# Kernel tuning notes

Measured on AMD Instinct MI355X. Metric: run time of the kernel, lower is better.

The kernel has to match this reference:

```python
import jax, jax.numpy as jnp
import numpy as np

# dims mirroring the torch module: dim=32 (MVN), omega=8, d_head=n_embd//n_head
B, T, E, DH = 8, 2048, 1024, 32
OMEGA, DIM = 8, 32
M = OMEGA * DIM  # 256 random features (omega concatenated N(0, I_dim) samples)


def setup_inputs() -> dict:
    key = jax.random.key(0)
    ks = jax.random.split(key, 8)
    s = 1.0 / np.sqrt(E).astype(np.float32)  # torch Linear-like init scale
    return {
        "x": jax.random.normal(ks[0], (B, T, E), jnp.float32),
        "Wq": jax.random.normal(ks[1], (E, DH), jnp.float32) * s,
        "bq": jax.random.normal(ks[2], (DH,), jnp.float32) * s,
        "Wk": jax.random.normal(ks[3], (E, DH), jnp.float32) * s,
        "bk": jax.random.normal(ks[4], (DH,), jnp.float32) * s,
        "Wv": jax.random.normal(ks[5], (E, DH), jnp.float32) * s,
        "bv": jax.random.normal(ks[6], (DH,), jnp.float32) * s,
        # random-feature matrix: omega stacked samples from N(0, I_DIM) -> [M, DH]
        "w": jax.random.normal(ks[7], (M, DH), jnp.float32),
    }


def reference(x, Wq, bq, Wk, bk, Wv, bv, w):
    # projections (as in Head.forward)
    q = x @ Wq + bq  # [B,T,DH]
    k = x @ Wk + bk  # [B,T,DH]
    v = x @ Wv + bv  # computed but unused, exactly as in the source
    del v
    # Aprox_softmax (FAVOR+-style hyperbolic random features), vectorized per token
    z = k + q                                          # [B,T,DH]
    zsqr = jnp.sum(k * k, -1) + jnp.sum(q * q, -1)     # [B,T]  (per-token norms)
    A = jnp.exp(-0.5 * zsqr)                           # [B,T]
    cosH = jnp.cosh(jnp.einsum('btd,md->btm', z, w))   # [B,T,M]
    R = A[..., None] * cosH                            # [B,T,M]
    return R
```

## Files before the change

### kernel.cpp

```cpp
#include <hip/hip_runtime.h>
#include <cstdint>

#define E_DIM   1024
#define DH      32
#define M_FEAT  256
#define BT      16384

typedef __attribute__((ext_vector_type(8))) short bf16x8;
typedef __attribute__((ext_vector_type(4))) float f32x4;

#define WP_H_OFF 0
#define WP_L_OFF (64*1024)
#define WF_H_OFF (2*64*1024)
#define WF_L_OFF (2*64*1024 + 256*32)

__device__ __forceinline__ void split_bf16(float f, short& h, short& l) {
    unsigned u = __builtin_bit_cast(unsigned, f);
    unsigned hr = (u + 0x7FFFu + ((u >> 16) & 1u)) & 0xFFFF0000u;
    h = (short)(hr >> 16);
    float fh = __builtin_bit_cast(float, hr);
    float d = f - fh;
    unsigned v = __builtin_bit_cast(unsigned, d);
    l = (short)((v + 0x7FFFu + ((v >> 16) & 1u)) >> 16);
}

__device__ __forceinline__ unsigned pack2(short a, short b) {
    return ((unsigned)(unsigned short)a) | (((unsigned)(unsigned short)b) << 16);
}

__global__ __launch_bounds__(256) void k_prep(
    const float* __restrict__ Wq, const float* __restrict__ Wk,
    const float* __restrict__ w, short* __restrict__ ws)
{
    int idx = blockIdx.x * 256 + threadIdx.x;
    short h[4], l[4];
    if (idx < 16384) {
        int n = idx >> 8, kq = idx & 255;
        const float* src = (n < 32) ? (Wq + n) : (Wk + (n - 32));
#pragma unroll
        for (int j = 0; j < 4; ++j) split_bf16(src[(kq * 4 + j) * DH], h[j], l[j]);
        uint2 ph = make_uint2(pack2(h[0], h[1]), pack2(h[2], h[3]));
        uint2 pl = make_uint2(pack2(l[0], l[1]), pack2(l[2], l[3]));
        *(uint2*)(ws + WP_H_OFF + n * 1024 + kq * 4) = ph;
        *(uint2*)(ws + WP_L_OFF + n * 1024 + kq * 4) = pl;
    } else if (idx < 16384 + 2048) {
        int j2 = idx - 16384;
        int n = j2 >> 3, kq = j2 & 7;
#pragma unroll
        for (int j = 0; j < 4; ++j) split_bf16(w[n * DH + kq * 4 + j], h[j], l[j]);
        uint2 ph = make_uint2(pack2(h[0], h[1]), pack2(h[2], h[3]));
        uint2 pl = make_uint2(pack2(l[0], l[1]), pack2(l[2], l[3]));
        *(uint2*)(ws + WF_H_OFF + n * DH + kq * 4) = ph;
        *(uint2*)(ws + WF_L_OFF + n * DH + kq * 4) = pl;
    }
}

#define XS 72
#define QS 68
#define ZS 40

__global__ __launch_bounds__(256) void k_main(
    const float* __restrict__ x, const float* __restrict__ bq,
    const float* __restrict__ bk, const short* __restrict__ ws,
    float* __restrict__ out)
{
    __shared__ __align__(16) short xh_s[32 * XS];
    __shared__ __align__(16) short xl_s[32 * XS];
    __shared__ __align__(16) float qk_f[32 * QS];
    __shared__ __align__(16) short zh_s[32 * ZS];
    __shared__ __align__(16) short zl_s[32 * ZS];
    __shared__ float lnA_f[32];

    const int tid  = threadIdx.x;
    const int lane = tid & 63;
    const int wv   = __builtin_amdgcn_readfirstlane(tid >> 6);
    const int ln15 = lane & 15;
    const int g    = lane >> 4;
    const long t0  = (long)blockIdx.x * 32;

    const short* wp_h = ws + WP_H_OFF;
    const short* wp_l = ws + WP_L_OFF;
    const short* wf_h = ws + WF_H_OFF;
    const short* wf_l = ws + WF_L_OFF;

    const int kq = tid & 15;
    const int mr = tid >> 4;

    f32x4 acc0 = {0.f, 0.f, 0.f, 0.f};
    f32x4 acc1 = {0.f, 0.f, 0.f, 0.f};

    const int nrow = wv * 16 + ln15;

    float4 st0 = *(const float4*)(x + (t0 + mr) * E_DIM + kq * 4);
    float4 st1 = *(const float4*)(x + (t0 + mr + 16) * E_DIM + kq * 4);

    for (int c = 0; c < 16; ++c) {
        __syncthreads();
        {
            short h0,h1,h2,h3, l0,l1,l2,l3;
            split_bf16(st0.x,h0,l0); split_bf16(st0.y,h1,l1);
            split_bf16(st0.z,h2,l2); split_bf16(st0.w,h3,l3);
            *(uint2*)&xh_s[mr * XS + kq * 4] = make_uint2(pack2(h0,h1), pack2(h2,h3));
            *(uint2*)&xl_s[mr * XS + kq * 4] = make_uint2(pack2(l0,l1), pack2(l2,l3));
            split_bf16(st1.x,h0,l0); split_bf16(st1.y,h1,l1);
            split_bf16(st1.z,h2,l2); split_bf16(st1.w,h3,l3);
            *(uint2*)&xh_s[(mr+16) * XS + kq * 4] = make_uint2(pack2(h0,h1), pack2(h2,h3));
            *(uint2*)&xl_s[(mr+16) * XS + kq * 4] = make_uint2(pack2(l0,l1), pack2(l2,l3));
        }
        __syncthreads();
        if (c < 15) {
            st0 = *(const float4*)(x + (t0 + mr) * E_DIM + (c+1)*64 + kq * 4);
            st1 = *(const float4*)(x + (t0 + mr + 16) * E_DIM + (c+1)*64 + kq * 4);
        }
#pragma unroll
        for (int s = 0; s < 2; ++s) {
            const int kb = c * 64 + s * 32;
            bf16x8 bh = *(const bf16x8*)(wp_h + nrow * 1024 + kb + g * 8);
            bf16x8 bl = *(const bf16x8*)(wp_l + nrow * 1024 + kb + g * 8);
            bf16x8 a0h = *(const bf16x8*)&xh_s[ln15 * XS + s * 32 + g * 8];
            bf16x8 a0l = *(const bf16x8*)&xl_s[ln15 * XS + s * 32 + g * 8];
            bf16x8 a1h = *(const bf16x8*)&xh_s[(ln15 + 16) * XS + s * 32 + g * 8];
            bf16x8 a1l = *(const bf16x8*)&xl_s[(ln15 + 16) * XS + s * 32 + g * 8];
            acc0 = __builtin_amdgcn_mfma_f32_16x16x32_bf16(a0h, bh, acc0, 0, 0, 0);
            acc0 = __builtin_amdgcn_mfma_f32_16x16x32_bf16(a0h, bl, acc0, 0, 0, 0);
            acc0 = __builtin_amdgcn_mfma_f32_16x16x32_bf16(a0l, bh, acc0, 0, 0, 0);
            acc1 = __builtin_amdgcn_mfma_f32_16x16x32_bf16(a1h, bh, acc1, 0, 0, 0);
            acc1 = __builtin_amdgcn_mfma_f32_16x16x32_bf16(a1h, bl, acc1, 0, 0, 0);
            acc1 = __builtin_amdgcn_mfma_f32_16x16x32_bf16(a1l, bh, acc1, 0, 0, 0);
        }
    }

    {
        const float bias = (nrow < 32) ? bq[nrow] : bk[nrow - 32];
#pragma unroll
        for (int r = 0; r < 4; ++r) {
            qk_f[(g * 4 + r) * QS + nrow]      = acc0[r] + bias;
            qk_f[(16 + g * 4 + r) * QS + nrow] = acc1[r] + bias;
        }
    }
    __syncthreads();

    {
        const int tok = tid >> 3, grp = tid & 7;
        float4 qv = *(const float4*)&qk_f[tok * QS + grp * 4];
        float4 kv = *(const float4*)&qk_f[tok * QS + 32 + grp * 4];
        float z0 = qv.x + kv.x, z1 = qv.y + kv.y, z2 = qv.z + kv.z, z3 = qv.w + kv.w;
        float p = qv.x*qv.x + qv.y*qv.y + qv.z*qv.z + qv.w*qv.w
                + kv.x*kv.x + kv.y*kv.y + kv.z*kv.z + kv.w*kv.w;
        short h0,h1,h2,h3, l0,l1,l2,l3;
        split_bf16(z0,h0,l0); split_bf16(z1,h1,l1);
        split_bf16(z2,h2,l2); split_bf16(z3,h3,l3);
        *(uint2*)&zh_s[tok * ZS + grp * 4] = make_uint2(pack2(h0,h1), pack2(h2,h3));
        *(uint2*)&zl_s[tok * ZS + grp * 4] = make_uint2(pack2(l0,l1), pack2(l2,l3));
        p += __shfl_xor(p, 1);
        p += __shfl_xor(p, 2);
        p += __shfl_xor(p, 4);
        if (grp == 0) lnA_f[tok] = -0.5f * p;
    }
    __syncthreads();

    f32x4 facc[4][2];
#pragma unroll
    for (int i = 0; i < 4; ++i)
#pragma unroll
        for (int mt = 0; mt < 2; ++mt) facc[i][mt] = (f32x4){0.f,0.f,0.f,0.f};

    bf16x8 a_h[2], a_l[2];
#pragma unroll
    for (int mt = 0; mt < 2; ++mt) {
        a_h[mt] = *(const bf16x8*)&zh_s[(mt * 16 + ln15) * ZS + g * 8];
        a_l[mt] = *(const bf16x8*)&zl_s[(mt * 16 + ln15) * ZS + g * 8];
    }
#pragma unroll
    for (int i = 0; i < 4; ++i) {
        const int nf = (wv * 4 + i) * 16 + ln15;
        bf16x8 bh = *(const bf16x8*)(wf_h + nf * DH + g * 8);
        bf16x8 bl = *(const bf16x8*)(wf_l + nf * DH + g * 8);
#pragma unroll
        for (int mt = 0; mt < 2; ++mt) {
            facc[i][mt] = __builtin_amdgcn_mfma_f32_16x16x32_bf16(a_h[mt], bh, facc[i][mt], 0, 0, 0);
            facc[i][mt] = __builtin_amdgcn_mfma_f32_16x16x32_bf16(a_h[mt], bl, facc[i][mt], 0, 0, 0);
            facc[i][mt] = __builtin_amdgcn_mfma_f32_16x16x32_bf16(a_l[mt], bh, facc[i][mt], 0, 0, 0);
        }
    }

    float lnAv[2][4];
#pragma unroll
    for (int mt = 0; mt < 2; ++mt)
#pragma unroll
        for (int r = 0; r < 4; ++r) lnAv[mt][r] = lnA_f[mt * 16 + g * 4 + r];

#pragma unroll
    for (int i = 0; i < 4; ++i) {
        const int n = (wv * 4 + i) * 16 + ln15;
#pragma unroll
        for (int mt = 0; mt < 2; ++mt) {
#pragma unroll
            for (int r = 0; r < 4; ++r) {
                float s = facc[i][mt][r];
                float R = 0.5f * (__expf(lnAv[mt][r] + s) + __expf(lnAv[mt][r] - s));
                out[(t0 + mt * 16 + g * 4 + r) * M_FEAT + n] = R;
            }
        }
    }
}

extern "C" void kernel_launch(void* const* d_in, const int* in_sizes, int n_in,
                              void* d_out, int out_size, void* d_ws, size_t ws_size,
                              hipStream_t stream) {
    const float* x  = (const float*)d_in[0];
    const float* Wq = (const float*)d_in[1];
    const float* bq = (const float*)d_in[2];
    const float* Wk = (const float*)d_in[3];
    const float* bk = (const float*)d_in[4];
    const float* w  = (const float*)d_in[7];
    float* out = (float*)d_out;
    short* ws  = (short*)d_ws;

    k_prep<<<dim3(72), dim3(256), 0, stream>>>(Wq, Wk, w, ws);
    k_main<<<dim3(BT / 32), dim3(256), 0, stream>>>(x, bq, bk, ws, out);
}
```

Baseline: 132.9 us.

## Halve token tile, double-buffer x in LDS, pre-swizzle weights into MFMA fragment layout

The main kernel now processes 16 tokens per block instead of 32, which doubles the grid to 1024 blocks. The x tile is double-buffered in shared memory, so one barrier per chunk is dropped and the bf16 split of the next chunk runs after the MFMAs. The prep kernel transposes the projection weights through LDS and writes them in per-lane fragment order, so each wave reads B fragments as contiguous coalesced 16-byte loads. The trade-off is that each block now re-reads the full projection weights for only 16 tokens, doubling weight traffic per token.

```diff
diff --git a/kernel.cpp b/kernel.cpp
--- a/kernel.cpp
+++ b/kernel.cpp
@@ -10,9 +10,9 @@
 typedef __attribute__((ext_vector_type(4))) float f32x4;
 
 #define WP_H_OFF 0
-#define WP_L_OFF (64*1024)
-#define WF_H_OFF (2*64*1024)
-#define WF_L_OFF (2*64*1024 + 256*32)
+#define WP_L_OFF 65536
+#define WF_H_OFF 131072
+#define WF_L_OFF (131072 + 8192)
 
 __device__ __forceinline__ void split_bf16(float f, short& h, short& l) {
     unsigned u = __builtin_bit_cast(unsigned, f);
@@ -32,29 +32,52 @@
     const float* __restrict__ Wq, const float* __restrict__ Wk,
     const float* __restrict__ w, short* __restrict__ ws)
 {
-    int idx = blockIdx.x * 256 + threadIdx.x;
-    short h[4], l[4];
-    if (idx < 16384) {
-        int n = idx >> 8, kq = idx & 255;
-        const float* src = (n < 32) ? (Wq + n) : (Wk + (n - 32));
-#pragma unroll
-        for (int j = 0; j < 4; ++j) split_bf16(src[(kq * 4 + j) * DH], h[j], l[j]);
-        uint2 ph = make_uint2(pack2(h[0], h[1]), pack2(h[2], h[3]));
-        uint2 pl = make_uint2(pack2(l[0], l[1]), pack2(l[2], l[3]));
-        *(uint2*)(ws + WP_H_OFF + n * 1024 + kq * 4) = ph;
-        *(uint2*)(ws + WP_L_OFF + n * 1024 + kq * 4) = pl;
-    } else if (idx < 16384 + 2048) {
-        int j2 = idx - 16384;
-        int n = j2 >> 3, kq = j2 & 7;
-#pragma unroll
-        for (int j = 0; j < 4; ++j) split_bf16(w[n * DH + kq * 4 + j], h[j], l[j]);
-        uint2 ph = make_uint2(pack2(h[0], h[1]), pack2(h[2], h[3]));
-        uint2 pl = make_uint2(pack2(l[0], l[1]), pack2(l[2], l[3]));
-        *(uint2*)(ws + WF_H_OFF + n * DH + kq * 4) = ph;
-        *(uint2*)(ws + WF_L_OFF + n * DH + kq * 4) = pl;
-    }
-}
-
+    __shared__ float wlds[128 * 36];
+    const int b = blockIdx.x, tid = threadIdx.x;
+    if (b < 16) {
+        const float* __restrict__ src = (b < 8) ? Wq : Wk;
+        const int k0 = (b & 7) * 128;
+        const int nbase = (b < 8) ? 0 : 32;
+#pragma unroll
+        for (int it = 0; it < 4; ++it) {
+            int f = it * 256 + tid;
+            int k = f >> 3, c4 = f & 7;
+            float4 v = *(const float4*)(src + (size_t)(k0 + k) * DH + c4 * 4);
+            *(float4*)&wlds[k * 36 + c4 * 4] = v;
+        }
+        __syncthreads();
+        const int n = tid >> 3, kq = tid & 7;
+        const int n_g = nbase + n;
+        const int nt = n_g >> 4, ln = n_g & 15;
+#pragma unroll
+        for (int rep = 0; rep < 4; ++rep) {
+            int kk = rep * 8 + kq;
+            int k_g = k0 + kk * 4;
+            short h[4], l[4];
+#pragma unroll
+            for (int j = 0; j < 4; ++j)
+                split_bf16(wlds[(kk * 4 + j) * 36 + n], h[j], l[j]);
+            int c = k_g >> 6, s = (k_g >> 5) & 1, g = (k_g >> 3) & 3, j0 = k_g & 7;
+            int lane = g * 16 + ln;
+            size_t flat = ((size_t)((nt * 16 + c) * 2 + s)) * 512 + lane * 8 + j0;
+            *(uint2*)(ws + WP_H_OFF + flat) = make_uint2(pack2(h[0],h[1]), pack2(h[2],h[3]));
+            *(uint2*)(ws + WP_L_OFF + flat) = make_uint2(pack2(l[0],l[1]), pack2(l[2],l[3]));
+        }
+    } else {
+#pragma unroll
+        for (int it = 0; it < 8; ++it) {
+            int f = it * 256 + tid;
+            float4 v = *(const float4*)(w + (size_t)f * 4);
+            short h[4], l[4];
+            split_bf16(v.x,h[0],l[0]); split_bf16(v.y,h[1],l[1]);
+            split_bf16(v.z,h[2],l[2]); split_bf16(v.w,h[3],l[3]);
+            *(uint2*)(ws + WF_H_OFF + f * 4) = make_uint2(pack2(h[0],h[1]), pack2(h[2],h[3]));
+            *(uint2*)(ws + WF_L_OFF + f * 4) = make_uint2(pack2(l[0],l[1]), pack2(l[2],l[3]));
+        }
+    }
+}
+
+#define TB 16
 #define XS 72
 #define QS 68
 #define ZS 40
@@ -64,83 +87,68 @@
     const float* __restrict__ bk, const short* __restrict__ ws,
     float* __restrict__ out)
 {
-    __shared__ __align__(16) short xh_s[32 * XS];
-    __shared__ __align__(16) short xl_s[32 * XS];
-    __shared__ __align__(16) float qk_f[32 * QS];
-    __shared__ __align__(16) short zh_s[32 * ZS];
-    __shared__ __align__(16) short zl_s[32 * ZS];
-    __shared__ float lnA_f[32];
+    __shared__ __align__(16) short xh_s[2][TB * XS];
+    __shared__ __align__(16) short xl_s[2][TB * XS];
+    __shared__ __align__(16) float qk_f[TB * QS];
+    __shared__ __align__(16) short zh_s[TB * ZS];
+    __shared__ __align__(16) short zl_s[TB * ZS];
+    __shared__ float lnA_f[TB];
 
     const int tid  = threadIdx.x;
     const int lane = tid & 63;
     const int wv   = __builtin_amdgcn_readfirstlane(tid >> 6);
     const int ln15 = lane & 15;
     const int g    = lane >> 4;
-    const long t0  = (long)blockIdx.x * 32;
-
-    const short* wp_h = ws + WP_H_OFF;
-    const short* wp_l = ws + WP_L_OFF;
-    const short* wf_h = ws + WF_H_OFF;
-    const short* wf_l = ws + WF_L_OFF;
+    const long t0  = (long)blockIdx.x * TB;
 
     const int kq = tid & 15;
     const int mr = tid >> 4;
 
-    f32x4 acc0 = {0.f, 0.f, 0.f, 0.f};
-    f32x4 acc1 = {0.f, 0.f, 0.f, 0.f};
-
-    const int nrow = wv * 16 + ln15;
-
-    float4 st0 = *(const float4*)(x + (t0 + mr) * E_DIM + kq * 4);
-    float4 st1 = *(const float4*)(x + (t0 + mr + 16) * E_DIM + kq * 4);
+    f32x4 acc = {0.f, 0.f, 0.f, 0.f};
+
+    float4 st = *(const float4*)(x + (t0 + mr) * E_DIM + kq * 4);
+    {
+        short h0,h1,h2,h3, l0,l1,l2,l3;
+        split_bf16(st.x,h0,l0); split_bf16(st.y,h1,l1);
+        split_bf16(st.z,h2,l2); split_bf16(st.w,h3,l3);
+        *(uint2*)&xh_s[0][mr * XS + kq * 4] = make_uint2(pack2(h0,h1), pack2(h2,h3));
+        *(uint2*)&xl_s[0][mr * XS + kq * 4] = make_uint2(pack2(l0,l1), pack2(l2,l3));
+    }
 
     for (int c = 0; c < 16; ++c) {
         __syncthreads();
-        {
+        if (c < 15)
+            st = *(const float4*)(x + (t0 + mr) * E_DIM + (c + 1) * 64 + kq * 4);
+#pragma unroll
+        for (int s = 0; s < 2; ++s) {
+            size_t fb = ((size_t)((wv * 16 + c) * 2 + s)) * 512 + lane * 8;
+            bf16x8 bh = *(const bf16x8*)(ws + WP_H_OFF + fb);
+            bf16x8 bl = *(const bf16x8*)(ws + WP_L_OFF + fb);
+            bf16x8 ah = *(const bf16x8*)&xh_s[c & 1][ln15 * XS + s * 32 + g * 8];
+            bf16x8 al = *(const bf16x8*)&xl_s[c & 1][ln15 * XS + s * 32 + g * 8];
+            acc = __builtin_amdgcn_mfma_f32_16x16x32_bf16(ah, bh, acc, 0, 0, 0);
+            acc = __builtin_amdgcn_mfma_f32_16x16x32_bf16(ah, bl, acc, 0, 0, 0);
+            acc = __builtin_amdgcn_mfma_f32_16x16x32_bf16(al, bh, acc, 0, 0, 0);
+        }
+        if (c < 15) {
             short h0,h1,h2,h3, l0,l1,l2,l3;
-            split_bf16(st0.x,h0,l0); split_bf16(st0.y,h1,l1);
-            split_bf16(st0.z,h2,l2); split_bf16(st0.w,h3,l3);
-            *(uint2*)&xh_s[mr * XS + kq * 4] = make_uint2(pack2(h0,h1), pack2(h2,h3));
-            *(uint2*)&xl_s[mr * XS + kq * 4] = make_uint2(pack2(l0,l1), pack2(l2,l3));
-            split_bf16(st1.x,h0,l0); split_bf16(st1.y,h1,l1);
-            split_bf16(st1.z,h2,l2); split_bf16(st1.w,h3,l3);
-            *(uint2*)&xh_s[(mr+16) * XS + kq * 4] = make_uint2(pack2(h0,h1), pack2(h2,h3));
-            *(uint2*)&xl_s[(mr+16) * XS + kq * 4] = make_uint2(pack2(l0,l1), pack2(l2,l3));
-        }
-        __syncthreads();
-        if (c < 15) {
-            st0 = *(const float4*)(x + (t0 + mr) * E_DIM + (c+1)*64 + kq * 4);
-            st1 = *(const float4*)(x + (t0 + mr + 16) * E_DIM + (c+1)*64 + kq * 4);
-        }
-#pragma unroll
-        for (int s = 0; s < 2; ++s) {
-            const int kb = c * 64 + s * 32;
-            bf16x8 bh = *(const bf16x8*)(wp_h + nrow * 1024 + kb + g * 8);
-            bf16x8 bl = *(const bf16x8*)(wp_l + nrow * 1024 + kb + g * 8);
-            bf16x8 a0h = *(const bf16x8*)&xh_s[ln15 * XS + s * 32 + g * 8];
-            bf16x8 a0l = *(const bf16x8*)&xl_s[ln15 * XS + s * 32 + g * 8];
-            bf16x8 a1h = *(const bf16x8*)&xh_s[(ln15 + 16) * XS + s * 32 + g * 8];
-            bf16x8 a1l = *(const bf16x8*)&xl_s[(ln15 + 16) * XS + s * 32 + g * 8];
-            acc0 = __builtin_amdgcn_mfma_f32_16x16x32_bf16(a0h, bh, acc0, 0, 0, 0);
-            acc0 = __builtin_amdgcn_mfma_f32_16x16x32_bf16(a0h, bl, acc0, 0, 0, 0);
-            acc0 = __builtin_amdgcn_mfma_f32_16x16x32_bf16(a0l, bh, acc0, 0, 0, 0);
-            acc1 = __builtin_amdgcn_mfma_f32_16x16x32_bf16(a1h, bh, acc1, 0, 0, 0);
-            acc1 = __builtin_amdgcn_mfma_f32_16x16x32_bf16(a1h, bl, acc1, 0, 0, 0);
-            acc1 = __builtin_amdgcn_mfma_f32_16x16x32_bf16(a1l, bh, acc1, 0, 0, 0);
-        }
-    }
-
+            split_bf16(st.x,h0,l0); split_bf16(st.y,h1,l1);
+            split_bf16(st.z,h2,l2); split_bf16(st.w,h3,l3);
+            *(uint2*)&xh_s[(c + 1) & 1][mr * XS + kq * 4] = make_uint2(pack2(h0,h1), pack2(h2,h3));
+            *(uint2*)&xl_s[(c + 1) & 1][mr * XS + kq * 4] = make_uint2(pack2(l0,l1), pack2(l2,l3));
+        }
+    }
+
+    const int nrow = wv * 16 + ln15;
     {
         const float bias = (nrow < 32) ? bq[nrow] : bk[nrow - 32];
 #pragma unroll
-        for (int r = 0; r < 4; ++r) {
-            qk_f[(g * 4 + r) * QS + nrow]      = acc0[r] + bias;
-            qk_f[(16 + g * 4 + r) * QS + nrow] = acc1[r] + bias;
-        }
+        for (int r = 0; r < 4; ++r)
+            qk_f[(g * 4 + r) * QS + nrow] = acc[r] + bias;
     }
     __syncthreads();
 
-    {
+    if (tid < 128) {
         const int tok = tid >> 3, grp = tid & 7;
         float4 qv = *(const float4*)&qk_f[tok * QS + grp * 4];
         float4 kv = *(const float4*)&qk_f[tok * QS + 32 + grp * 4];
@@ -159,48 +167,34 @@
     }
     __syncthreads();
 
-    f32x4 facc[4][2];
-#pragma unroll
-    for (int i = 0; i < 4; ++i)
-#pragma unroll
-        for (int mt = 0; mt < 2; ++mt) facc[i][mt] = (f32x4){0.f,0.f,0.f,0.f};
-
-    bf16x8 a_h[2], a_l[2];
-#pragma unroll
-    for (int mt = 0; mt < 2; ++mt) {
-        a_h[mt] = *(const bf16x8*)&zh_s[(mt * 16 + ln15) * ZS + g * 8];
-        a_l[mt] = *(const bf16x8*)&zl_s[(mt * 16 + ln15) * ZS + g * 8];
-    }
+    f32x4 facc[4];
+#pragma unroll
+    for (int i = 0; i < 4; ++i) facc[i] = (f32x4){0.f,0.f,0.f,0.f};
+
+    bf16x8 a_h = *(const bf16x8*)&zh_s[ln15 * ZS + g * 8];
+    bf16x8 a_l = *(const bf16x8*)&zl_s[ln15 * ZS + g * 8];
 #pragma unroll
     for (int i = 0; i < 4; ++i) {
         const int nf = (wv * 4 + i) * 16 + ln15;
-        bf16x8 bh = *(const bf16x8*)(wf_h + nf * DH + g * 8);
-        bf16x8 bl = *(const bf16x8*)(wf_l + nf * DH + g * 8);
-#pragma unroll
-        for (int mt = 0; mt < 2; ++mt) {
-            facc[i][mt] = __builtin_amdgcn_mfma_f32_16x16x32_bf16(a_h[mt], bh, facc[i][mt], 0, 0, 0);
-            facc[i][mt] = __builtin_amdgcn_mfma_f32_16x16x32_bf16(a_h[mt], bl, facc[i][mt], 0, 0, 0);
-            facc[i][mt] = __builtin_amdgcn_mfma_f32_16x16x32_bf16(a_l[mt], bh, facc[i][mt], 0, 0, 0);
-        }
-    }
-
-    float lnAv[2][4];
-#pragma unroll
-    for (int mt = 0; mt < 2; ++mt)
-#pragma unroll
-        for (int r = 0; r < 4; ++r) lnAv[mt][r] = lnA_f[mt * 16 + g * 4 + r];
+        bf16x8 bh = *(const bf16x8*)(ws + WF_H_OFF + (size_t)nf * DH + g * 8);
+        bf16x8 bl = *(const bf16x8*)(ws + WF_L_OFF + (size_t)nf * DH + g * 8);
+        facc[i] = __builtin_amdgcn_mfma_f32_16x16x32_bf16(a_h, bh, facc[i], 0, 0, 0);
+        facc[i] = __builtin_amdgcn_mfma_f32_16x16x32_bf16(a_h, bl, facc[i], 0, 0, 0);
+        facc[i] = __builtin_amdgcn_mfma_f32_16x16x32_bf16(a_l, bh, facc[i], 0, 0, 0);
+    }
+
+    float lnAv[4];
+#pragma unroll
+    for (int r = 0; r < 4; ++r) lnAv[r] = lnA_f[g * 4 + r];
 
 #pragma unroll
     for (int i = 0; i < 4; ++i) {
         const int n = (wv * 4 + i) * 16 + ln15;
 #pragma unroll
-        for (int mt = 0; mt < 2; ++mt) {
-#pragma unroll
-            for (int r = 0; r < 4; ++r) {
-                float s = facc[i][mt][r];
-                float R = 0.5f * (__expf(lnAv[mt][r] + s) + __expf(lnAv[mt][r] - s));
-                out[(t0 + mt * 16 + g * 4 + r) * M_FEAT + n] = R;
-            }
+        for (int r = 0; r < 4; ++r) {
+            float s = facc[i][r];
+            float R = 0.5f * (__expf(lnAv[r] + s) + __expf(lnAv[r] - s));
+            out[(t0 + g * 4 + r) * M_FEAT + n] = R;
         }
     }
 }
@@ -217,6 +211,6 @@
     float* out = (float*)d_out;
     short* ws  = (short*)d_ws;
 
-    k_prep<<<dim3(72), dim3(256), 0, stream>>>(Wq, Wk, w, ws);
-    k_main<<<dim3(BT / 32), dim3(256), 0, stream>>>(x, bq, bk, ws, out);
-}
+    k_prep<<<dim3(17), dim3(256), 0, stream>>>(Wq, Wk, w, ws);
+    k_main<<<dim3(BT / TB), dim3(256), 0, stream>>>(x, bq, bk, ws, out);
+}
```

Result: faster. 127.5 us (-4.1%).
